# Performance work log

Measured on AMD Instinct MI355X. Metric: run time of the kernel, lower is better.

## Reference

```python
import jax, jax.numpy as jnp
import numpy as np


def setup_inputs() -> dict:
    key = jax.random.key(0)
    k1, k2 = jax.random.split(key)
    B, Tq, Ts, H = 16, 2048, 2048, 1024
    hidden = jax.random.normal(k1, (B, Tq, H), dtype=jnp.float32)
    encoder_outputs = jax.random.normal(k2, (B, Ts, H), dtype=jnp.float32)
    return {"hidden": hidden, "encoder_outputs": encoder_outputs}


def reference(hidden, encoder_outputs):
    # scores[b, s, q] = <encoder_outputs[b, s], hidden[b, q]>  (no scaling)
    scores = jnp.einsum("bsh,bqh->bsq", encoder_outputs, hidden)
    # softmax over the source dimension s (dim=1, the NON-last axis)
    attn_weights = jax.nn.softmax(scores, axis=1)
    # context[b, q, h] = sum_s attn[b, s, q] * enc[b, s, h]
    context = jnp.einsum("bsq,bsh->bqh", attn_weights, encoder_outputs)
    return context
```

## Files before the change

### kernel.cpp

```cpp
#include <hip/hip_runtime.h>

#define NB_ 16
#define TQ_ 2048
#define TS_ 2048
#define DH_ 1024
#define QB_ 32
#define SB_ 128
#define NT_ 512

typedef _Float16 f16x8 __attribute__((ext_vector_type(8)));
typedef _Float16 f16x4 __attribute__((ext_vector_type(4)));
typedef float f32x4 __attribute__((ext_vector_type(4)));

__device__ inline uint32_t pack_h2(float a, float b) {
  union { _Float16 h[2]; uint32_t u; } c;
  c.h[0] = (_Float16)a; c.h[1] = (_Float16)b;
  return c.u;
}

__global__ void convert_f32_f16(const float* __restrict__ src, _Float16* __restrict__ dst) {
  size_t i = ((size_t)blockIdx.x * blockDim.x + threadIdx.x) * 8;
  float4 v0 = *(const float4*)(src + i);
  float4 v1 = *(const float4*)(src + i + 4);
  f16x8 o;
  o[0] = (_Float16)v0.x; o[1] = (_Float16)v0.y; o[2] = (_Float16)v0.z; o[3] = (_Float16)v0.w;
  o[4] = (_Float16)v1.x; o[5] = (_Float16)v1.y; o[6] = (_Float16)v1.z; o[7] = (_Float16)v1.w;
  *(f16x8*)(dst + i) = o;
}

template<bool WS16>
__device__ inline f16x8 ld8(const _Float16* __restrict__ hp, const float* __restrict__ fp, size_t idx) {
  if constexpr (WS16) {
    return *(const f16x8*)(hp + idx);
  } else {
    float4 a = *(const float4*)(fp + idx);
    float4 b = *(const float4*)(fp + idx + 4);
    f16x8 t;
    t[0] = (_Float16)a.x; t[1] = (_Float16)a.y; t[2] = (_Float16)a.z; t[3] = (_Float16)a.w;
    t[4] = (_Float16)b.x; t[5] = (_Float16)b.y; t[6] = (_Float16)b.z; t[7] = (_Float16)b.w;
    return t;
  }
}

template<bool WS16>
__global__ __launch_bounds__(NT_, 2)
void attn_v8(const float* __restrict__ hid,
             const float* __restrict__ enc,
             const _Float16* __restrict__ encH,
             float* __restrict__ out) {
  __shared__ __attribute__((aligned(16))) char smem[156544];
  char*  const q_base = smem;
  float* const s_lds  = (float*)(smem + 65536);
  char*  const p_base = smem + 82432;
  char*  const vt_all = smem + 90624;
  float* const m_lds  = (float*)(smem + 156160);
  float* const l_lds  = m_lds + 32;
  float* const c_lds  = m_lds + 64;

  const int tid  = threadIdx.x;
  const int lane = tid & 63;
  const int wid  = tid >> 6;
  const int arow = lane & 15;
  const int agrp = lane >> 4;

  const int bi  = blockIdx.x;
  const int x   = bi & 7;
  const int idx = bi >> 3;
  const int b   = x + 8 * (idx >> 6);
  const int q0  = (idx & 63) * QB_;

  const int hw = wid;

  if (tid < 32) { m_lds[tid] = -__builtin_inff(); l_lds[tid] = 0.0f; }

  {
    const float* qsrc = hid + ((size_t)b * TQ_ + q0) * DH_;
    #pragma unroll
    for (int k = 0; k < 16; ++k) {
      int i = tid + k * NT_;
      int q = i >> 8;
      int h = (i & 255) * 4;
      float4 v = *(const float4*)(qsrc + (size_t)q * DH_ + h);
      int byte = (q * 2048 + h * 2) ^ ((q & 7) << 4);
      *(uint32_t*)(q_base + byte)     = pack_h2(v.x, v.y);
      *(uint32_t*)(q_base + byte + 4) = pack_h2(v.z, v.w);
    }
  }
  __syncthreads();

  f32x4 o_acc[2][8];
  #pragma unroll
  for (int m = 0; m < 2; ++m)
    #pragma unroll
    for (int n = 0; n < 8; ++n)
      o_acc[m][n] = {};

  char* const vt = vt_all + wid * 8192;
  const size_t enc_b = (size_t)b * TS_ * DH_;
  const int h8  = (lane & 15) * 8;
  const int spb = (lane >> 4) * 2;

  for (int st = 0; st < TS_ / SB_; ++st) {
    const int s0 = st * SB_;

    f32x4 sacc0 = {}, sacc1 = {};
    {
      const size_t krow = enc_b + (size_t)(s0 + wid * 16 + arow) * DH_;
      #pragma unroll
      for (int kf = 0; kf < 32; ++kf) {
        const int d = kf * 32 + agrp * 8;
        f16x8 bf  = ld8<WS16>(encH, enc, krow + d);
        f16x8 af0 = *(const f16x8*)(q_base + ((arow * 2048 + d * 2) ^ ((arow & 7) << 4)));
        f16x8 af1 = *(const f16x8*)(q_base + (((16 + arow) * 2048 + d * 2) ^ ((arow & 7) << 4)));
        sacc0 = __builtin_amdgcn_mfma_f32_16x16x32_f16(af0, bf, sacc0, 0, 0, 0);
        sacc1 = __builtin_amdgcn_mfma_f32_16x16x32_f16(af1, bf, sacc1, 0, 0, 0);
      }
    }

    f16x8 stg[4][2];
    #pragma unroll
    for (int it = 0; it < 4; ++it) {
      size_t base = enc_b + (size_t)(s0 + it * 8 + spb) * DH_ + hw * 128 + h8;
      stg[it][0] = ld8<WS16>(encH, enc, base);
      stg[it][1] = ld8<WS16>(encH, enc, base + DH_);
    }

    {
      const int sc = wid * 16 + arow;
      #pragma unroll
      for (int i2 = 0; i2 < 4; ++i2) {
        s_lds[(agrp * 4 + i2) * 132 + sc]        = sacc0[i2];
        s_lds[(16 + agrp * 4 + i2) * 132 + sc]   = sacc1[i2];
      }
    }

    __syncthreads();

    {
      int q = tid >> 4, sq = tid & 15;
      const float* bp = s_lds + q * 132 + sq * 4;
      f32x4 va = *(const f32x4*)bp;
      f32x4 vb = *(const f32x4*)(bp + 64);
      float mx = fmaxf(fmaxf(fmaxf(va[0], va[1]), fmaxf(va[2], va[3])),
                       fmaxf(fmaxf(vb[0], vb[1]), fmaxf(vb[2], vb[3])));
      #pragma unroll
      for (int o = 8; o; o >>= 1) mx = fmaxf(mx, __shfl_xor(mx, o));
      float mprev = m_lds[q];
      float mnew  = fmaxf(mprev, mx);
      float pa0 = __expf(va[0] - mnew), pa1 = __expf(va[1] - mnew);
      float pa2 = __expf(va[2] - mnew), pa3 = __expf(va[3] - mnew);
      float pb0 = __expf(vb[0] - mnew), pb1 = __expf(vb[1] - mnew);
      float pb2 = __expf(vb[2] - mnew), pb3 = __expf(vb[3] - mnew);
      float ps = ((pa0 + pa1) + (pa2 + pa3)) + ((pb0 + pb1) + (pb2 + pb3));
      #pragma unroll
      for (int o = 8; o; o >>= 1) ps += __shfl_xor(ps, o);
      if (sq == 0) {
        float cf = __expf(mprev - mnew);
        m_lds[q] = mnew;
        l_lds[q] = l_lds[q] * cf + ps;
        c_lds[q] = cf;
      }
      f16x4 pwa, pwb;
      pwa[0] = (_Float16)pa0; pwa[1] = (_Float16)pa1;
      pwa[2] = (_Float16)pa2; pwa[3] = (_Float16)pa3;
      pwb[0] = (_Float16)pb0; pwb[1] = (_Float16)pb1;
      pwb[2] = (_Float16)pb2; pwb[3] = (_Float16)pb3;
      *(f16x4*)(p_base + ((q * 256 + sq * 8) ^ ((q & 7) << 4)))       = pwa;
      *(f16x4*)(p_base + ((q * 256 + 128 + sq * 8) ^ ((q & 7) << 4))) = pwb;
    }

    __syncthreads();

    #pragma unroll
    for (int m = 0; m < 2; ++m)
      #pragma unroll
      for (int i2 = 0; i2 < 4; ++i2) {
        float cf = c_lds[m * 16 + agrp * 4 + i2];
        #pragma unroll
        for (int n = 0; n < 8; ++n) o_acc[m][n][i2] *= cf;
      }

    #pragma unroll
    for (int ph = 0; ph < 4; ++ph) {
      #pragma unroll
      for (int it = 0; it < 4; ++it) {
        int sp = it * 8 + spb;
        #pragma unroll
        for (int jj = 0; jj < 8; ++jj) {
          int hloc = h8 + jj;
          union { _Float16 h[2]; uint32_t u; } pk;
          pk.h[0] = stg[it][0][jj]; pk.h[1] = stg[it][1][jj];
          *(uint32_t*)(vt + ((hloc * 64 + sp * 2) ^ (((hloc >> 3) & 7) << 4))) = pk.u;
        }
      }
      if (ph < 3) {
        #pragma unroll
        for (int it = 0; it < 4; ++it) {
          size_t base = enc_b + (size_t)(s0 + (ph + 1) * 32 + it * 8 + spb) * DH_ + hw * 128 + h8;
          stg[it][0] = ld8<WS16>(encH, enc, base);
          stg[it][1] = ld8<WS16>(encH, enc, base + DH_);
        }
      }
      f16x8 paf0 = *(const f16x8*)(p_base +
          ((arow * 256 + ph * 64 + agrp * 16) ^ ((arow & 7) << 4)));
      f16x8 paf1 = *(const f16x8*)(p_base +
          (((16 + arow) * 256 + ph * 64 + agrp * 16) ^ ((arow & 7) << 4)));
      __builtin_amdgcn_s_setprio(1);
      #pragma unroll
      for (int n = 0; n < 8; ++n) {
        int hloc = n * 16 + arow;
        f16x8 bv = *(const f16x8*)(vt + ((hloc * 64 + agrp * 16) ^ (((hloc >> 3) & 7) << 4)));
        o_acc[0][n] = __builtin_amdgcn_mfma_f32_16x16x32_f16(paf0, bv, o_acc[0][n], 0, 0, 0);
        o_acc[1][n] = __builtin_amdgcn_mfma_f32_16x16x32_f16(paf1, bv, o_acc[1][n], 0, 0, 0);
      }
      __builtin_amdgcn_s_setprio(0);
    }
  }

  #pragma unroll
  for (int m = 0; m < 2; ++m) {
    #pragma unroll
    for (int i2 = 0; i2 < 4; ++i2) {
      int qr = m * 16 + agrp * 4 + i2;
      float inv = 1.0f / l_lds[qr];
      #pragma unroll
      for (int n = 0; n < 8; ++n) {
        out[((size_t)(b * TQ_ + q0 + qr)) * DH_ + hw * 128 + n * 16 + arow] =
            o_acc[m][n][i2] * inv;
      }
    }
  }
}

extern "C" void kernel_launch(void* const* d_in, const int* in_sizes, int n_in,
                              void* d_out, int out_size, void* d_ws, size_t ws_size,
                              hipStream_t stream) {
  (void)in_sizes; (void)n_in; (void)out_size;
  const float* hid = (const float*)d_in[0];
  const float* enc = (const float*)d_in[1];
  float* out = (float*)d_out;

  const size_t encN = (size_t)NB_ * TS_ * DH_;
  const bool ws16 = (ws_size >= encN * sizeof(_Float16));

  dim3 grid(NB_ * (TQ_ / QB_), 1, 1);
  dim3 block(NT_, 1, 1);

  if (ws16) {
    _Float16* encH = (_Float16*)d_ws;
    convert_f32_f16<<<dim3((unsigned)(encN / 8 / 256)), dim3(256), 0, stream>>>(enc, encH);
    attn_v8<true><<<grid, block, 0, stream>>>(hid, enc, encH, out);
  } else {
    attn_v8<false><<<grid, block, 0, stream>>>(hid, enc, nullptr, out);
  }
}
```

Baseline: 851.0 us.

## Hold Q fragments in registers and split the QK reduction over head-dim across waves

```diff
diff --git a/kernel.cpp b/kernel.cpp
--- a/kernel.cpp
+++ b/kernel.cpp
@@ -12,11 +12,7 @@
 typedef _Float16 f16x4 __attribute__((ext_vector_type(4)));
 typedef float f32x4 __attribute__((ext_vector_type(4)));
 
-__device__ inline uint32_t pack_h2(float a, float b) {
-  union { _Float16 h[2]; uint32_t u; } c;
-  c.h[0] = (_Float16)a; c.h[1] = (_Float16)b;
-  return c.u;
-}
+#define LDS_BARRIER() asm volatile("s_waitcnt lgkmcnt(0)\n\ts_barrier" ::: "memory")
 
 __global__ void convert_f32_f16(const float* __restrict__ src, _Float16* __restrict__ dst) {
   size_t i = ((size_t)blockIdx.x * blockDim.x + threadIdx.x) * 8;
@@ -28,34 +24,34 @@
   *(f16x8*)(dst + i) = o;
 }
 
+__device__ inline f16x8 cvt8(const float* __restrict__ fp) {
+  float4 a = *(const float4*)fp;
+  float4 b = *(const float4*)(fp + 4);
+  f16x8 t;
+  t[0] = (_Float16)a.x; t[1] = (_Float16)a.y; t[2] = (_Float16)a.z; t[3] = (_Float16)a.w;
+  t[4] = (_Float16)b.x; t[5] = (_Float16)b.y; t[6] = (_Float16)b.z; t[7] = (_Float16)b.w;
+  return t;
+}
+
 template<bool WS16>
 __device__ inline f16x8 ld8(const _Float16* __restrict__ hp, const float* __restrict__ fp, size_t idx) {
-  if constexpr (WS16) {
-    return *(const f16x8*)(hp + idx);
-  } else {
-    float4 a = *(const float4*)(fp + idx);
-    float4 b = *(const float4*)(fp + idx + 4);
-    f16x8 t;
-    t[0] = (_Float16)a.x; t[1] = (_Float16)a.y; t[2] = (_Float16)a.z; t[3] = (_Float16)a.w;
-    t[4] = (_Float16)b.x; t[5] = (_Float16)b.y; t[6] = (_Float16)b.z; t[7] = (_Float16)b.w;
-    return t;
-  }
+  if constexpr (WS16) return *(const f16x8*)(hp + idx);
+  else return cvt8(fp + idx);
 }
 
 template<bool WS16>
 __global__ __launch_bounds__(NT_, 2)
-void attn_v8(const float* __restrict__ hid,
-             const float* __restrict__ enc,
-             const _Float16* __restrict__ encH,
-             float* __restrict__ out) {
-  __shared__ __attribute__((aligned(16))) char smem[156544];
-  char*  const q_base = smem;
-  float* const s_lds  = (float*)(smem + 65536);
-  char*  const p_base = smem + 82432;
-  char*  const vt_all = smem + 90624;
-  float* const m_lds  = (float*)(smem + 156160);
-  float* const l_lds  = m_lds + 32;
-  float* const c_lds  = m_lds + 64;
+void attn_v10(const float* __restrict__ hid,
+              const float* __restrict__ enc,
+              const _Float16* __restrict__ encH,
+              float* __restrict__ out) {
+  __shared__ __attribute__((aligned(16))) char smem[143744];
+  char*  const vt_all  = smem;
+  float* const s_tiles = (float*)(smem + 65536);
+  char*  const p_base  = smem + 135168;
+  float* const m_lds   = (float*)(smem + 143360);
+  float* const l_lds   = m_lds + 32;
+  float* const c_lds   = m_lds + 64;
 
   const int tid  = threadIdx.x;
   const int lane = tid & 63;
@@ -69,24 +65,22 @@
   const int b   = x + 8 * (idx >> 6);
   const int q0  = (idx & 63) * QB_;
 
+  const int dw = wid & 3;
+  const int sh = wid >> 2;
   const int hw = wid;
 
   if (tid < 32) { m_lds[tid] = -__builtin_inff(); l_lds[tid] = 0.0f; }
 
-  {
-    const float* qsrc = hid + ((size_t)b * TQ_ + q0) * DH_;
-    #pragma unroll
-    for (int k = 0; k < 16; ++k) {
-      int i = tid + k * NT_;
-      int q = i >> 8;
-      int h = (i & 255) * 4;
-      float4 v = *(const float4*)(qsrc + (size_t)q * DH_ + h);
-      int byte = (q * 2048 + h * 2) ^ ((q & 7) << 4);
-      *(uint32_t*)(q_base + byte)     = pack_h2(v.x, v.y);
-      *(uint32_t*)(q_base + byte + 4) = pack_h2(v.z, v.w);
-    }
-  }
-  __syncthreads();
+  f16x8 a_q[2][8];
+  #pragma unroll
+  for (int m = 0; m < 2; ++m) {
+    #pragma unroll
+    for (int kf = 0; kf < 8; ++kf) {
+      const float* qp = hid + ((size_t)(b * TQ_ + q0 + m * 16 + arow)) * DH_
+                            + dw * 256 + kf * 32 + agrp * 8;
+      a_q[m][kf] = cvt8(qp);
+    }
+  }
 
   f32x4 o_acc[2][8];
   #pragma unroll
@@ -103,17 +97,20 @@
   for (int st = 0; st < TS_ / SB_; ++st) {
     const int s0 = st * SB_;
 
-    f32x4 sacc0 = {}, sacc1 = {};
-    {
-      const size_t krow = enc_b + (size_t)(s0 + wid * 16 + arow) * DH_;
-      #pragma unroll
-      for (int kf = 0; kf < 32; ++kf) {
-        const int d = kf * 32 + agrp * 8;
-        f16x8 bf  = ld8<WS16>(encH, enc, krow + d);
-        f16x8 af0 = *(const f16x8*)(q_base + ((arow * 2048 + d * 2) ^ ((arow & 7) << 4)));
-        f16x8 af1 = *(const f16x8*)(q_base + (((16 + arow) * 2048 + d * 2) ^ ((arow & 7) << 4)));
-        sacc0 = __builtin_amdgcn_mfma_f32_16x16x32_f16(af0, bf, sacc0, 0, 0, 0);
-        sacc1 = __builtin_amdgcn_mfma_f32_16x16x32_f16(af1, bf, sacc1, 0, 0, 0);
+    f32x4 sacc[2][4] = {{{}, {}, {}, {}}, {{}, {}, {}, {}}};
+    #pragma unroll
+    for (int kf = 0; kf < 8; ++kf) {
+      const int d = dw * 256 + kf * 32 + agrp * 8;
+      f16x8 bf[4];
+      #pragma unroll
+      for (int n = 0; n < 4; ++n) {
+        size_t kb = enc_b + (size_t)(s0 + sh * 64 + n * 16 + arow) * DH_ + d;
+        bf[n] = ld8<WS16>(encH, enc, kb);
+      }
+      #pragma unroll
+      for (int n = 0; n < 4; ++n) {
+        sacc[0][n] = __builtin_amdgcn_mfma_f32_16x16x32_f16(a_q[0][kf], bf[n], sacc[0][n], 0, 0, 0);
+        sacc[1][n] = __builtin_amdgcn_mfma_f32_16x16x32_f16(a_q[1][kf], bf[n], sacc[1][n], 0, 0, 0);
       }
     }
 
@@ -126,21 +123,30 @@
     }
 
     {
-      const int sc = wid * 16 + arow;
-      #pragma unroll
-      for (int i2 = 0; i2 < 4; ++i2) {
-        s_lds[(agrp * 4 + i2) * 132 + sc]        = sacc0[i2];
-        s_lds[(16 + agrp * 4 + i2) * 132 + sc]   = sacc1[i2];
-      }
-    }
-
-    __syncthreads();
+      float* tp = s_tiles + (size_t)(sh * 4 + dw) * (32 * 68);
+      #pragma unroll
+      for (int m = 0; m < 2; ++m)
+        #pragma unroll
+        for (int n = 0; n < 4; ++n)
+          #pragma unroll
+          for (int i2 = 0; i2 < 4; ++i2)
+            tp[(m * 16 + agrp * 4 + i2) * 68 + n * 16 + arow] = sacc[m][n][i2];
+    }
+
+    LDS_BARRIER();
 
     {
       int q = tid >> 4, sq = tid & 15;
-      const float* bp = s_lds + q * 132 + sq * 4;
+      const float* bp = s_tiles + q * 68 + sq * 4;
       f32x4 va = *(const f32x4*)bp;
-      f32x4 vb = *(const f32x4*)(bp + 64);
+      va += *(const f32x4*)(bp + 2176);
+      va += *(const f32x4*)(bp + 4352);
+      va += *(const f32x4*)(bp + 6528);
+      const float* bq = bp + 8704;
+      f32x4 vb = *(const f32x4*)bq;
+      vb += *(const f32x4*)(bq + 2176);
+      vb += *(const f32x4*)(bq + 4352);
+      vb += *(const f32x4*)(bq + 6528);
       float mx = fmaxf(fmaxf(fmaxf(va[0], va[1]), fmaxf(va[2], va[3])),
                        fmaxf(fmaxf(vb[0], vb[1]), fmaxf(vb[2], vb[3])));
       #pragma unroll
@@ -169,7 +175,7 @@
       *(f16x4*)(p_base + ((q * 256 + 128 + sq * 8) ^ ((q & 7) << 4))) = pwb;
     }
 
-    __syncthreads();
+    LDS_BARRIER();
 
     #pragma unroll
     for (int m = 0; m < 2; ++m)
@@ -249,8 +255,8 @@
   if (ws16) {
     _Float16* encH = (_Float16*)d_ws;
     convert_f32_f16<<<dim3((unsigned)(encN / 8 / 256)), dim3(256), 0, stream>>>(enc, encH);
-    attn_v8<true><<<grid, block, 0, stream>>>(hid, enc, encH, out);
+    attn_v10<true><<<grid, block, 0, stream>>>(hid, enc, encH, out);
   } else {
-    attn_v8<false><<<grid, block, 0, stream>>>(hid, enc, nullptr, out);
-  }
-}
+    attn_v10<false><<<grid, block, 0, stream>>>(hid, enc, nullptr, out);
+  }
+}
```

Result: no change. 866.7 us (+1.8%).

## Double source tile to 256 and double-buffer V staging with half-width passes

Applied to the files above, without the earlier changes.

```diff
diff --git a/kernel.cpp b/kernel.cpp
--- a/kernel.cpp
+++ b/kernel.cpp
@@ -5,7 +5,7 @@
 #define TS_ 2048
 #define DH_ 1024
 #define QB_ 32
-#define SB_ 128
+#define SB_ 256
 #define NT_ 512
 
 typedef _Float16 f16x8 __attribute__((ext_vector_type(8)));
@@ -28,32 +28,33 @@
   *(f16x8*)(dst + i) = o;
 }
 
+__device__ inline f16x8 cvt8(const float* __restrict__ fp) {
+  float4 a = *(const float4*)fp;
+  float4 b = *(const float4*)(fp + 4);
+  f16x8 t;
+  t[0] = (_Float16)a.x; t[1] = (_Float16)a.y; t[2] = (_Float16)a.z; t[3] = (_Float16)a.w;
+  t[4] = (_Float16)b.x; t[5] = (_Float16)b.y; t[6] = (_Float16)b.z; t[7] = (_Float16)b.w;
+  return t;
+}
+
 template<bool WS16>
 __device__ inline f16x8 ld8(const _Float16* __restrict__ hp, const float* __restrict__ fp, size_t idx) {
-  if constexpr (WS16) {
-    return *(const f16x8*)(hp + idx);
-  } else {
-    float4 a = *(const float4*)(fp + idx);
-    float4 b = *(const float4*)(fp + idx + 4);
-    f16x8 t;
-    t[0] = (_Float16)a.x; t[1] = (_Float16)a.y; t[2] = (_Float16)a.z; t[3] = (_Float16)a.w;
-    t[4] = (_Float16)b.x; t[5] = (_Float16)b.y; t[6] = (_Float16)b.z; t[7] = (_Float16)b.w;
-    return t;
-  }
+  if constexpr (WS16) return *(const f16x8*)(hp + idx);
+  else return cvt8(fp + idx);
 }
 
 template<bool WS16>
 __global__ __launch_bounds__(NT_, 2)
-void attn_v8(const float* __restrict__ hid,
-             const float* __restrict__ enc,
-             const _Float16* __restrict__ encH,
-             float* __restrict__ out) {
-  __shared__ __attribute__((aligned(16))) char smem[156544];
+void attn_v12(const float* __restrict__ hid,
+              const float* __restrict__ enc,
+              const _Float16* __restrict__ encH,
+              float* __restrict__ out) {
+  __shared__ __attribute__((aligned(16))) char smem[148352];
   char*  const q_base = smem;
   float* const s_lds  = (float*)(smem + 65536);
-  char*  const p_base = smem + 82432;
-  char*  const vt_all = smem + 90624;
-  float* const m_lds  = (float*)(smem + 156160);
+  char*  const p_base = smem + 98816;
+  char*  const vt_all = smem + 115200;
+  float* const m_lds  = (float*)(smem + 147968);
   float* const l_lds  = m_lds + 32;
   float* const c_lds  = m_lds + 64;
 
@@ -95,63 +96,77 @@
     for (int n = 0; n < 8; ++n)
       o_acc[m][n] = {};
 
-  char* const vt = vt_all + wid * 8192;
+  char* const vt = vt_all + wid * 4096;
   const size_t enc_b = (size_t)b * TS_ * DH_;
-  const int h8  = (lane & 15) * 8;
-  const int spb = (lane >> 4) * 2;
+  const int c8 = (lane & 7) * 8;
+  const int d2 = (lane >> 3) * 2;
 
   for (int st = 0; st < TS_ / SB_; ++st) {
     const int s0 = st * SB_;
 
-    f32x4 sacc0 = {}, sacc1 = {};
+    f32x4 sacc[2][2] = {{{}, {}}, {{}, {}}};
     {
-      const size_t krow = enc_b + (size_t)(s0 + wid * 16 + arow) * DH_;
+      const size_t krow = enc_b + (size_t)(s0 + wid * 32 + arow) * DH_;
       #pragma unroll
       for (int kf = 0; kf < 32; ++kf) {
         const int d = kf * 32 + agrp * 8;
-        f16x8 bf  = ld8<WS16>(encH, enc, krow + d);
+        f16x8 bf0 = ld8<WS16>(encH, enc, krow + d);
+        f16x8 bf1 = ld8<WS16>(encH, enc, krow + (size_t)16 * DH_ + d);
         f16x8 af0 = *(const f16x8*)(q_base + ((arow * 2048 + d * 2) ^ ((arow & 7) << 4)));
         f16x8 af1 = *(const f16x8*)(q_base + (((16 + arow) * 2048 + d * 2) ^ ((arow & 7) << 4)));
-        sacc0 = __builtin_amdgcn_mfma_f32_16x16x32_f16(af0, bf, sacc0, 0, 0, 0);
-        sacc1 = __builtin_amdgcn_mfma_f32_16x16x32_f16(af1, bf, sacc1, 0, 0, 0);
-      }
-    }
-
-    f16x8 stg[4][2];
-    #pragma unroll
-    for (int it = 0; it < 4; ++it) {
-      size_t base = enc_b + (size_t)(s0 + it * 8 + spb) * DH_ + hw * 128 + h8;
-      stg[it][0] = ld8<WS16>(encH, enc, base);
-      stg[it][1] = ld8<WS16>(encH, enc, base + DH_);
+        sacc[0][0] = __builtin_amdgcn_mfma_f32_16x16x32_f16(af0, bf0, sacc[0][0], 0, 0, 0);
+        sacc[0][1] = __builtin_amdgcn_mfma_f32_16x16x32_f16(af0, bf1, sacc[0][1], 0, 0, 0);
+        sacc[1][0] = __builtin_amdgcn_mfma_f32_16x16x32_f16(af1, bf0, sacc[1][0], 0, 0, 0);
+        sacc[1][1] = __builtin_amdgcn_mfma_f32_16x16x32_f16(af1, bf1, sacc[1][1], 0, 0, 0);
+      }
+    }
+
+    f16x8 stgA[2][2], stgB[2][2];
+    #pragma unroll
+    for (int it = 0; it < 2; ++it) {
+      size_t base = enc_b + (size_t)(s0 + it * 16 + d2) * DH_ + hw * 128 + c8;
+      stgA[it][0] = ld8<WS16>(encH, enc, base);
+      stgA[it][1] = ld8<WS16>(encH, enc, base + DH_);
     }
 
     {
-      const int sc = wid * 16 + arow;
-      #pragma unroll
-      for (int i2 = 0; i2 < 4; ++i2) {
-        s_lds[(agrp * 4 + i2) * 132 + sc]        = sacc0[i2];
-        s_lds[(16 + agrp * 4 + i2) * 132 + sc]   = sacc1[i2];
-      }
+      const int sc = wid * 32 + arow;
+      #pragma unroll
+      for (int m = 0; m < 2; ++m)
+        #pragma unroll
+        for (int n = 0; n < 2; ++n)
+          #pragma unroll
+          for (int i2 = 0; i2 < 4; ++i2)
+            s_lds[(m * 16 + agrp * 4 + i2) * 260 + sc + n * 16] = sacc[m][n][i2];
     }
 
     __syncthreads();
 
     {
       int q = tid >> 4, sq = tid & 15;
-      const float* bp = s_lds + q * 132 + sq * 4;
-      f32x4 va = *(const f32x4*)bp;
-      f32x4 vb = *(const f32x4*)(bp + 64);
-      float mx = fmaxf(fmaxf(fmaxf(va[0], va[1]), fmaxf(va[2], va[3])),
-                       fmaxf(fmaxf(vb[0], vb[1]), fmaxf(vb[2], vb[3])));
+      const float* bp = s_lds + q * 260 + sq * 16;
+      f32x4 v0 = *(const f32x4*)bp;
+      f32x4 v1 = *(const f32x4*)(bp + 4);
+      f32x4 v2 = *(const f32x4*)(bp + 8);
+      f32x4 v3 = *(const f32x4*)(bp + 12);
+      f32x4 vm = v0;
+      #pragma unroll
+      for (int j = 0; j < 4; ++j) { vm[j] = fmaxf(fmaxf(v0[j], v1[j]), fmaxf(v2[j], v3[j])); }
+      float mx = fmaxf(fmaxf(vm[0], vm[1]), fmaxf(vm[2], vm[3]));
       #pragma unroll
       for (int o = 8; o; o >>= 1) mx = fmaxf(mx, __shfl_xor(mx, o));
       float mprev = m_lds[q];
       float mnew  = fmaxf(mprev, mx);
-      float pa0 = __expf(va[0] - mnew), pa1 = __expf(va[1] - mnew);
-      float pa2 = __expf(va[2] - mnew), pa3 = __expf(va[3] - mnew);
-      float pb0 = __expf(vb[0] - mnew), pb1 = __expf(vb[1] - mnew);
-      float pb2 = __expf(vb[2] - mnew), pb3 = __expf(vb[3] - mnew);
-      float ps = ((pa0 + pa1) + (pa2 + pa3)) + ((pb0 + pb1) + (pb2 + pb3));
+      float p[16], ps = 0.0f;
+      #pragma unroll
+      for (int j = 0; j < 4; ++j) {
+        p[j]      = __expf(v0[j] - mnew);
+        p[4 + j]  = __expf(v1[j] - mnew);
+        p[8 + j]  = __expf(v2[j] - mnew);
+        p[12 + j] = __expf(v3[j] - mnew);
+      }
+      #pragma unroll
+      for (int j = 0; j < 16; ++j) ps += p[j];
       #pragma unroll
       for (int o = 8; o; o >>= 1) ps += __shfl_xor(ps, o);
       if (sq == 0) {
@@ -160,13 +175,13 @@
         l_lds[q] = l_lds[q] * cf + ps;
         c_lds[q] = cf;
       }
-      f16x4 pwa, pwb;
-      pwa[0] = (_Float16)pa0; pwa[1] = (_Float16)pa1;
-      pwa[2] = (_Float16)pa2; pwa[3] = (_Float16)pa3;
-      pwb[0] = (_Float16)pb0; pwb[1] = (_Float16)pb1;
-      pwb[2] = (_Float16)pb2; pwb[3] = (_Float16)pb3;
-      *(f16x4*)(p_base + ((q * 256 + sq * 8) ^ ((q & 7) << 4)))       = pwa;
-      *(f16x4*)(p_base + ((q * 256 + 128 + sq * 8) ^ ((q & 7) << 4))) = pwb;
+      #pragma unroll
+      for (int g = 0; g < 4; ++g) {
+        f16x4 pw;
+        pw[0] = (_Float16)p[g * 4 + 0]; pw[1] = (_Float16)p[g * 4 + 1];
+        pw[2] = (_Float16)p[g * 4 + 2]; pw[3] = (_Float16)p[g * 4 + 3];
+        *(f16x4*)(p_base + ((q * 512 + sq * 32 + g * 8) ^ ((q & 7) << 4))) = pw;
+      }
     }
 
     __syncthreads();
@@ -181,37 +196,47 @@
       }
 
     #pragma unroll
-    for (int ph = 0; ph < 4; ++ph) {
-      #pragma unroll
-      for (int it = 0; it < 4; ++it) {
-        int sp = it * 8 + spb;
+    for (int pass = 0; pass < 16; ++pass) {
+      const int r  = pass >> 3, sp = pass & 7;
+      const bool useA = (pass & 1) == 0;
+      #pragma unroll
+      for (int it = 0; it < 2; ++it) {
+        int sl = it * 16 + d2;
         #pragma unroll
         for (int jj = 0; jj < 8; ++jj) {
-          int hloc = h8 + jj;
+          int hl = c8 + jj;
           union { _Float16 h[2]; uint32_t u; } pk;
-          pk.h[0] = stg[it][0][jj]; pk.h[1] = stg[it][1][jj];
-          *(uint32_t*)(vt + ((hloc * 64 + sp * 2) ^ (((hloc >> 3) & 7) << 4))) = pk.u;
+          pk.h[0] = useA ? stgA[it][0][jj] : stgB[it][0][jj];
+          pk.h[1] = useA ? stgA[it][1][jj] : stgB[it][1][jj];
+          *(uint32_t*)(vt + ((hl * 64 + sl * 2) ^ (((hl >> 3) & 7) << 4))) = pk.u;
         }
       }
-      if (ph < 3) {
-        #pragma unroll
-        for (int it = 0; it < 4; ++it) {
-          size_t base = enc_b + (size_t)(s0 + (ph + 1) * 32 + it * 8 + spb) * DH_ + hw * 128 + h8;
-          stg[it][0] = ld8<WS16>(encH, enc, base);
-          stg[it][1] = ld8<WS16>(encH, enc, base + DH_);
+      if (pass < 15) {
+        const int rn = (pass + 1) >> 3, spn = (pass + 1) & 7;
+        #pragma unroll
+        for (int it = 0; it < 2; ++it) {
+          size_t base = enc_b + (size_t)(s0 + spn * 32 + it * 16 + d2) * DH_
+                        + hw * 128 + rn * 64 + c8;
+          if (useA) {
+            stgB[it][0] = ld8<WS16>(encH, enc, base);
+            stgB[it][1] = ld8<WS16>(encH, enc, base + DH_);
+          } else {
+            stgA[it][0] = ld8<WS16>(encH, enc, base);
+            stgA[it][1] = ld8<WS16>(encH, enc, base + DH_);
+          }
         }
       }
       f16x8 paf0 = *(const f16x8*)(p_base +
-          ((arow * 256 + ph * 64 + agrp * 16) ^ ((arow & 7) << 4)));
+          ((arow * 512 + sp * 64 + agrp * 16) ^ ((arow & 7) << 4)));
       f16x8 paf1 = *(const f16x8*)(p_base +
-          (((16 + arow) * 256 + ph * 64 + agrp * 16) ^ ((arow & 7) << 4)));
+          (((16 + arow) * 512 + sp * 64 + agrp * 16) ^ ((arow & 7) << 4)));
       __builtin_amdgcn_s_setprio(1);
       #pragma unroll
-      for (int n = 0; n < 8; ++n) {
-        int hloc = n * 16 + arow;
-        f16x8 bv = *(const f16x8*)(vt + ((hloc * 64 + agrp * 16) ^ (((hloc >> 3) & 7) << 4)));
-        o_acc[0][n] = __builtin_amdgcn_mfma_f32_16x16x32_f16(paf0, bv, o_acc[0][n], 0, 0, 0);
-        o_acc[1][n] = __builtin_amdgcn_mfma_f32_16x16x32_f16(paf1, bv, o_acc[1][n], 0, 0, 0);
+      for (int n = 0; n < 4; ++n) {
+        int hl = n * 16 + arow;
+        f16x8 bv = *(const f16x8*)(vt + ((hl * 64 + agrp * 16) ^ (((hl >> 3) & 7) << 4)));
+        o_acc[0][r * 4 + n] = __builtin_amdgcn_mfma_f32_16x16x32_f16(paf0, bv, o_acc[0][r * 4 + n], 0, 0, 0);
+        o_acc[1][r * 4 + n] = __builtin_amdgcn_mfma_f32_16x16x32_f16(paf1, bv, o_acc[1][r * 4 + n], 0, 0, 0);
       }
       __builtin_amdgcn_s_setprio(0);
     }
@@ -225,7 +250,7 @@
       float inv = 1.0f / l_lds[qr];
       #pragma unroll
       for (int n = 0; n < 8; ++n) {
-        out[((size_t)(b * TQ_ + q0 + qr)) * DH_ + hw * 128 + n * 16 + arow] =
+        out[((size_t)(b * TQ_ + q0 + qr)) * DH_ + hw * 128 + (n >> 2) * 64 + (n & 3) * 16 + arow] =
             o_acc[m][n][i2] * inv;
       }
     }
@@ -249,8 +274,8 @@
   if (ws16) {
     _Float16* encH = (_Float16*)d_ws;
     convert_f32_f16<<<dim3((unsigned)(encN / 8 / 256)), dim3(256), 0, stream>>>(enc, encH);
-    attn_v8<true><<<grid, block, 0, stream>>>(hid, enc, encH, out);
+    attn_v12<true><<<grid, block, 0, stream>>>(hid, enc, encH, out);
   } else {
-    attn_v8<false><<<grid, block, 0, stream>>>(hid, enc, nullptr, out);
-  }
-}
+    attn_v12<false><<<grid, block, 0, stream>>>(hid, enc, nullptr, out);
+  }
+}
```

Measured after the change: 741.9 us. 1.15x faster.
